# Performance work log

Measured on AMD Instinct MI355X. Metric: run time of the kernel, lower is better.

## Reference

```python
import jax, jax.numpy as jnp
import numpy as np


def _lstm_layer(x_seq, w_ih, w_hh, b_ih, b_hh):
    """One LSTM layer, batch_first x_seq [B,T,D]; PyTorch gate order i,f,g,o."""
    B, T, _ = x_seq.shape
    H = w_hh.shape[1]
    # precompute input contribution for all timesteps: [B,T,4H]
    xg = jnp.einsum('btd,gd->btg', x_seq, w_ih) + b_ih + b_hh
    xg_t = jnp.swapaxes(xg, 0, 1)  # [T,B,4H]

    def step(carry, g_in):
        h, c = carry
        g = g_in + h @ w_hh.T  # [B,4H]
        i, f, gg, o = jnp.split(g, 4, axis=-1)
        i = jax.nn.sigmoid(i)
        f = jax.nn.sigmoid(f)
        gg = jnp.tanh(gg)
        o = jax.nn.sigmoid(o)
        c = f * c + i * gg
        h = o * jnp.tanh(c)
        return (h, c), h

    h0 = jnp.zeros((B, H), x_seq.dtype)
    c0 = jnp.zeros((B, H), x_seq.dtype)
    (_, _), hs = jax.lax.scan(step, (h0, c0), xg_t)
    return jnp.swapaxes(hs, 0, 1)  # [B,T,H]


def setup_inputs() -> dict:
    key = jax.random.key(0)
    ks = jax.random.split(key, 12)
    V, E, H, B, T = 50000, 100, 64, 256, 512
    s = 0.1
    emb = jax.random.normal(ks[0], (V, E), jnp.float32) * s
    emb = emb.at[0].set(0.0)  # padding_idx=0
    return {
        'x': jax.random.randint(ks[1], (B, T), 0, V),
        'emb': emb,
        'w_ih0': jax.random.normal(ks[2], (4 * H, E), jnp.float32) * s,
        'w_hh0': jax.random.normal(ks[3], (4 * H, H), jnp.float32) * s,
        'b_ih0': jax.random.normal(ks[4], (4 * H,), jnp.float32) * s,
        'b_hh0': jax.random.normal(ks[5], (4 * H,), jnp.float32) * s,
        'w_ih1': jax.random.normal(ks[6], (4 * H, H), jnp.float32) * s,
        'w_hh1': jax.random.normal(ks[7], (4 * H, H), jnp.float32) * s,
        'b_ih1': jax.random.normal(ks[8], (4 * H,), jnp.float32) * s,
        'b_hh1': jax.random.normal(ks[9], (4 * H,), jnp.float32) * s,
        'fc_w': jax.random.normal(ks[10], (1, H), jnp.float32) * s,
        'fc_b': jax.random.normal(ks[11], (1,), jnp.float32) * s,
    }


def reference(x, emb, w_ih0, w_hh0, b_ih0, b_hh0,
              w_ih1, w_hh1, b_ih1, b_hh1, fc_w, fc_b):
    emb_eff = emb.at[0].set(0.0)  # padding_idx=0 row stays zero
    embedded = emb_eff[x]  # [B,T,E]
    h1 = _lstm_layer(embedded, w_ih0, w_hh0, b_ih0, b_hh0)
    h2 = _lstm_layer(h1, w_ih1, w_hh1, b_ih1, b_hh1)
    last = h2[:, -1, :]  # [B,H]
    # eval mode: dropout is identity
    act = jax.nn.relu(last)
    out = act @ fc_w.T + fc_b  # [B,1]
    return jax.nn.sigmoid(out)
```

## Files before the change

kernel.cpp:

```cpp
#include <hip/hip_runtime.h>

#define VSZ 50000
#define ESZ 100
#define HSZ 64
#define GSZ 256
#define BSZ 256
#define TSZ 512

__device__ __forceinline__ float fast_rcp(float x) { return __builtin_amdgcn_rcpf(x); }
__device__ __forceinline__ float sigmoid_f(float x) { return fast_rcp(1.f + __expf(-x)); }
__device__ __forceinline__ float tanh_f(float x) {
    float e = __expf(2.f * x);
    return 1.f - 2.f * fast_rcp(e + 1.f);
}

__global__ __launch_bounds__(256) void build_table(
    const float* __restrict__ emb, const float* __restrict__ w_ih0,
    const float* __restrict__ b_ih0, const float* __restrict__ b_hh0,
    float* __restrict__ Gt)
{
    const int g = threadIdx.x;
    const int row0 = blockIdx.x * 32;
    const int col = ((g & 63) << 2) + (g >> 6);

    float w[ESZ];
    #pragma unroll
    for (int e = 0; e < ESZ; e += 4) {
        float4 v = *(const float4*)(w_ih0 + g * ESZ + e);
        w[e] = v.x; w[e + 1] = v.y; w[e + 2] = v.z; w[e + 3] = v.w;
    }
    const float bias = b_ih0[g] + b_hh0[g];

    #pragma unroll 1
    for (int r = row0; r < row0 + 32 && r < VSZ; r += 2) {
        const int off0 = __builtin_amdgcn_readfirstlane(r * ESZ);
        const float* e0 = emb + off0;
        const float* e1 = e0 + ESZ;
        float a0 = bias, a1 = 0.f, a2 = 0.f, a3 = 0.f;
        float b0 = bias, b1 = 0.f, b2 = 0.f, b3 = 0.f;
        #pragma unroll
        for (int e = 0; e < ESZ; e += 4) {
            a0 += e0[e    ] * w[e    ]; a1 += e0[e + 1] * w[e + 1];
            a2 += e0[e + 2] * w[e + 2]; a3 += e0[e + 3] * w[e + 3];
            b0 += e1[e    ] * w[e    ]; b1 += e1[e + 1] * w[e + 1];
            b2 += e1[e + 2] * w[e + 2]; b3 += e1[e + 3] * w[e + 3];
        }
        Gt[(size_t)r       * GSZ + col] = (a0 + a1) + (a2 + a3);
        Gt[(size_t)(r + 1) * GSZ + col] = (b0 + b1) + (b2 + b3);
    }
}

__device__ __forceinline__ void sync_lds() {
    asm volatile("s_waitcnt lgkmcnt(0)\n\ts_barrier" ::: "memory");
}

#define LD4(ptr, off) (*(const float4*)((ptr) + (off)))
#define K4(v) asm volatile("" : "+v"(v.x), "+v"(v.y), "+v"(v.z), "+v"(v.w))
#define KEEPALL \
  K4(W00);K4(W01);K4(W02);K4(W03);K4(W10);K4(W11);K4(W12);K4(W13); \
  K4(W20);K4(W21);K4(W22);K4(W23);K4(W30);K4(W31);K4(W32);K4(W33); \
  K4(U00);K4(U01);K4(U02);K4(U03);K4(U10);K4(U11);K4(U12);K4(U13); \
  K4(U20);K4(U21);K4(U22);K4(U23);K4(U30);K4(U31);K4(U32);K4(U33)
#define DOTACC(p, W, h) p += W.x*h.x; p += W.y*h.y; p += W.z*h.z; p += W.w*h.w

__global__ __launch_bounds__(512, 2) void lstm_fused(
    const int* __restrict__ x, const float* __restrict__ Gt,
    const float* __restrict__ w_hh0,
    const float* __restrict__ w_ih1, const float* __restrict__ w_hh1,
    const float* __restrict__ b_ih1, const float* __restrict__ b_hh1,
    const float* __restrict__ fc_w, const float* __restrict__ fc_b,
    float* __restrict__ out)
{
    const int tid = threadIdx.x;
    const int b   = blockIdx.x;
    const bool isA = tid < 256;
    const int lt  = tid & 255;
    const int q   = lt >> 2;
    const int j   = lt & 3;

    __shared__ __align__(16) float h0b[2][HSZ];
    __shared__ __align__(16) float h1b[2][HSZ];
    __shared__ int xtok[TSZ];

    const float* bW = (isA ? w_hh0 : w_ih1) + (q * HSZ + 16 * j);
    const float* bU = w_hh1 + (q * HSZ + 16 * j);

    float4 W00=LD4(bW,0),     W01=LD4(bW,4),     W02=LD4(bW,8),     W03=LD4(bW,12);
    float4 W10=LD4(bW,4096),  W11=LD4(bW,4100),  W12=LD4(bW,4104),  W13=LD4(bW,4108);
    float4 W20=LD4(bW,8192),  W21=LD4(bW,8196),  W22=LD4(bW,8200),  W23=LD4(bW,8204);
    float4 W30=LD4(bW,12288), W31=LD4(bW,12292), W32=LD4(bW,12296), W33=LD4(bW,12300);
    float4 U00=LD4(bU,0),     U01=LD4(bU,4),     U02=LD4(bU,8),     U03=LD4(bU,12);
    float4 U10=LD4(bU,4096),  U11=LD4(bU,4100),  U12=LD4(bU,4104),  U13=LD4(bU,4108);
    float4 U20=LD4(bU,8192),  U21=LD4(bU,8196),  U22=LD4(bU,8200),  U23=LD4(bU,8204);
    float4 U30=LD4(bU,12288), U31=LD4(bU,12292), U32=LD4(bU,12296), U33=LD4(bU,12300);

    float bi0 = 0.f, bi1 = 0.f, bi2 = 0.f, bi3 = 0.f;
    if (!isA) {
        bi0 = b_ih1[q]       + b_hh1[q];
        bi1 = b_ih1[64 + q]  + b_hh1[64 + q];
        bi2 = b_ih1[128 + q] + b_hh1[128 + q];
        bi3 = b_ih1[192 + q] + b_hh1[192 + q];
    }

    if (tid < 128)      ((float*)h0b)[tid] = 0.f;
    else if (tid < 256) ((float*)h1b)[tid - 128] = 0.f;
    xtok[tid] = x[b * TSZ + tid];
    __syncthreads();

    float4 xg = LD4(Gt, (size_t)xtok[0] * GSZ + 4 * q);
    float c = 0.f;

    #pragma unroll 1
    for (int k = 0; k <= TSZ; ++k) {
        KEEPALL;

        const int rb = (k ^ 1) & 1;
        const float4* h0v = (const float4*)h0b[rb];
        float4 ha = h0v[j*4+0], hb = h0v[j*4+1], hc = h0v[j*4+2], hd = h0v[j*4+3];
        float p0 = 0.f, p1 = 0.f, p2 = 0.f, p3 = 0.f;
        DOTACC(p0,W00,ha); DOTACC(p0,W01,hb); DOTACC(p0,W02,hc); DOTACC(p0,W03,hd);
        DOTACC(p1,W10,ha); DOTACC(p1,W11,hb); DOTACC(p1,W12,hc); DOTACC(p1,W13,hd);
        DOTACC(p2,W20,ha); DOTACC(p2,W21,hb); DOTACC(p2,W22,hc); DOTACC(p2,W23,hd);
        DOTACC(p3,W30,ha); DOTACC(p3,W31,hb); DOTACC(p3,W32,hc); DOTACC(p3,W33,hd);

        if (!isA && k >= 1) {
            const float4* h1v = (const float4*)h1b[k & 1];
            float4 ea = h1v[j*4+0], eb = h1v[j*4+1], ec = h1v[j*4+2], ed = h1v[j*4+3];
            DOTACC(p0,U00,ea); DOTACC(p0,U01,eb); DOTACC(p0,U02,ec); DOTACC(p0,U03,ed);
            DOTACC(p1,U10,ea); DOTACC(p1,U11,eb); DOTACC(p1,U12,ec); DOTACC(p1,U13,ed);
            DOTACC(p2,U20,ea); DOTACC(p2,U21,eb); DOTACC(p2,U22,ec); DOTACC(p2,U23,ed);
            DOTACC(p3,U30,ea); DOTACC(p3,U31,eb); DOTACC(p3,U32,ec); DOTACC(p3,U33,ed);
        }

        p0 += __shfl_xor(p0, 1, 64); p0 += __shfl_xor(p0, 2, 64);
        p1 += __shfl_xor(p1, 1, 64); p1 += __shfl_xor(p1, 2, 64);
        p2 += __shfl_xor(p2, 1, 64); p2 += __shfl_xor(p2, 2, 64);
        p3 += __shfl_xor(p3, 1, 64); p3 += __shfl_xor(p3, 2, 64);

        if (isA) {
            if (k < TSZ) {
                float4 xg_n;
                const bool pf = (k + 1 < TSZ);
                if (pf) xg_n = LD4(Gt, (size_t)xtok[k + 1] * GSZ + 4 * q);
                float ig = sigmoid_f(p0 + xg.x);
                float fg = sigmoid_f(p1 + xg.y);
                float gg = tanh_f   (p2 + xg.z);
                float og = sigmoid_f(p3 + xg.w);
                c = fg * c + ig * gg;
                float hn = og * tanh_f(c);
                if (j == 0) h0b[k & 1][q] = hn;
                if (pf) xg = xg_n;
            }
        } else {
            if (k >= 1) {
                float ig = sigmoid_f(p0 + bi0);
                float fg = sigmoid_f(p1 + bi1);
                float gg = tanh_f   (p2 + bi2);
                float og = sigmoid_f(p3 + bi3);
                c = fg * c + ig * gg;
                float hn = og * tanh_f(c);
                if (j == 0) h1b[(k ^ 1) & 1][q] = hn;
            }
        }
        sync_lds();
    }

    if (tid < HSZ) {
        float v = fmaxf(h1b[1][tid], 0.f) * fc_w[tid];
        #pragma unroll
        for (int off = 32; off > 0; off >>= 1) v += __shfl_down(v, off, 64);
        if (tid == 0) out[b] = sigmoid_f(v + fc_b[0]);
    }
}

extern "C" void kernel_launch(void* const* d_in, const int* in_sizes, int n_in,
                              void* d_out, int out_size, void* d_ws, size_t ws_size,
                              hipStream_t stream) {
    const int*   x     = (const int*)  d_in[0];
    const float* emb   = (const float*)d_in[1];
    const float* w_ih0 = (const float*)d_in[2];
    const float* w_hh0 = (const float*)d_in[3];
    const float* b_ih0 = (const float*)d_in[4];
    const float* b_hh0 = (const float*)d_in[5];
    const float* w_ih1 = (const float*)d_in[6];
    const float* w_hh1 = (const float*)d_in[7];
    const float* b_ih1 = (const float*)d_in[8];
    const float* b_hh1 = (const float*)d_in[9];
    const float* fc_w  = (const float*)d_in[10];
    const float* fc_b  = (const float*)d_in[11];
    float* out = (float*)d_out;

    float* Gt = (float*)d_ws;

    build_table<<<dim3((VSZ + 31) / 32), dim3(256), 0, stream>>>(
        emb, w_ih0, b_ih0, b_hh0, Gt);
    lstm_fused<<<dim3(BSZ), dim3(512), 0, stream>>>(
        x, Gt, w_hh0, w_ih1, w_hh1, b_ih1, b_hh1, fc_w, fc_b, out);
}
```

Before: 568.4 us.

## Split layer-1 work across 512 threads and distribute gate activations per lane

The fused LSTM kernel grows from 512 to 768 threads. The layer-1 group now uses 8 lanes per hidden unit, each holding half the weights, which cuts per-thread registers and FMA chain length. Each lane now evaluates one gate activation through a unified sigmoid/tanh formula after a butterfly reduction, instead of every lane computing all four. The table-building kernel switches to float4 embedding loads and a different occupancy bound. The cost is extra shuffles per step and larger blocks, which may limit occupancy.

```diff
diff --git a/kernel.cpp b/kernel.cpp
--- a/kernel.cpp
+++ b/kernel.cpp
@@ -14,7 +14,7 @@
     return 1.f - 2.f * fast_rcp(e + 1.f);
 }
 
-__global__ __launch_bounds__(256) void build_table(
+__global__ __launch_bounds__(256, 2) void build_table(
     const float* __restrict__ emb, const float* __restrict__ w_ih0,
     const float* __restrict__ b_ih0, const float* __restrict__ b_hh0,
     float* __restrict__ Gt)
@@ -32,18 +32,23 @@
     const float bias = b_ih0[g] + b_hh0[g];
 
     #pragma unroll 1
-    for (int r = row0; r < row0 + 32 && r < VSZ; r += 2) {
-        const int off0 = __builtin_amdgcn_readfirstlane(r * ESZ);
-        const float* e0 = emb + off0;
+    for (int r = row0; r < row0 + 32; r += 2) {
+        if (r + 1 >= VSZ + 1) break;
+        if (r >= VSZ) break;
+        unsigned long long u0 = (unsigned long long)(emb + (size_t)r * ESZ);
+        asm("" : "+v"(u0));
+        const float* e0 = (const float*)u0;
         const float* e1 = e0 + ESZ;
         float a0 = bias, a1 = 0.f, a2 = 0.f, a3 = 0.f;
         float b0 = bias, b1 = 0.f, b2 = 0.f, b3 = 0.f;
         #pragma unroll
         for (int e = 0; e < ESZ; e += 4) {
-            a0 += e0[e    ] * w[e    ]; a1 += e0[e + 1] * w[e + 1];
-            a2 += e0[e + 2] * w[e + 2]; a3 += e0[e + 3] * w[e + 3];
-            b0 += e1[e    ] * w[e    ]; b1 += e1[e + 1] * w[e + 1];
-            b2 += e1[e + 2] * w[e + 2]; b3 += e1[e + 3] * w[e + 3];
+            float4 u = *(const float4*)(e0 + e);
+            float4 v = *(const float4*)(e1 + e);
+            a0 += u.x * w[e]; a1 += u.y * w[e + 1];
+            a2 += u.z * w[e + 2]; a3 += u.w * w[e + 3];
+            b0 += v.x * w[e]; b1 += v.y * w[e + 1];
+            b2 += v.z * w[e + 2]; b3 += v.w * w[e + 3];
         }
         Gt[(size_t)r       * GSZ + col] = (a0 + a1) + (a2 + a3);
         Gt[(size_t)(r + 1) * GSZ + col] = (b0 + b1) + (b2 + b3);
@@ -55,15 +60,14 @@
 }
 
 #define LD4(ptr, off) (*(const float4*)((ptr) + (off)))
-#define K4(v) asm volatile("" : "+v"(v.x), "+v"(v.y), "+v"(v.z), "+v"(v.w))
-#define KEEPALL \
-  K4(W00);K4(W01);K4(W02);K4(W03);K4(W10);K4(W11);K4(W12);K4(W13); \
-  K4(W20);K4(W21);K4(W22);K4(W23);K4(W30);K4(W31);K4(W32);K4(W33); \
-  K4(U00);K4(U01);K4(U02);K4(U03);K4(U10);K4(U11);K4(U12);K4(U13); \
-  K4(U20);K4(U21);K4(U22);K4(U23);K4(U30);K4(U31);K4(U32);K4(U33)
-#define DOTACC(p, W, h) p += W.x*h.x; p += W.y*h.y; p += W.z*h.z; p += W.w*h.w
-
-__global__ __launch_bounds__(512, 2) void lstm_fused(
+#define PIN4(v) asm("" : "+v"(v.x), "+v"(v.y), "+v"(v.z), "+v"(v.w))
+#define DOT4(acc, Sa, Sb, Sc, Sd)                                  \
+    acc += Sa.x*H0.x; acc += Sa.y*H0.y; acc += Sa.z*H0.z; acc += Sa.w*H0.w; \
+    acc += Sb.x*H1.x; acc += Sb.y*H1.y; acc += Sb.z*H1.z; acc += Sb.w*H1.w; \
+    acc += Sc.x*H2.x; acc += Sc.y*H2.y; acc += Sc.z*H2.z; acc += Sc.w*H2.w; \
+    acc += Sd.x*H3.x; acc += Sd.y*H3.y; acc += Sd.z*H3.z; acc += Sd.w*H3.w
+
+__global__ __launch_bounds__(768, 3) void lstm_fused(
     const int* __restrict__ x, const float* __restrict__ Gt,
     const float* __restrict__ w_hh0,
     const float* __restrict__ w_ih1, const float* __restrict__ w_hh1,
@@ -74,94 +78,99 @@
     const int tid = threadIdx.x;
     const int b   = blockIdx.x;
     const bool isA = tid < 256;
-    const int lt  = tid & 255;
-    const int q   = lt >> 2;
-    const int j   = lt & 3;
+    const int lt  = isA ? tid : (tid - 256);
+    const int q   = isA ? (lt >> 2) : (lt >> 3);
+    const int j   = isA ? (lt & 3) : (lt & 7);
+    const int gt  = j & 3;
 
     __shared__ __align__(16) float h0b[2][HSZ];
     __shared__ __align__(16) float h1b[2][HSZ];
     __shared__ int xtok[TSZ];
 
-    const float* bW = (isA ? w_hh0 : w_ih1) + (q * HSZ + 16 * j);
-    const float* bU = w_hh1 + (q * HSZ + 16 * j);
-
-    float4 W00=LD4(bW,0),     W01=LD4(bW,4),     W02=LD4(bW,8),     W03=LD4(bW,12);
-    float4 W10=LD4(bW,4096),  W11=LD4(bW,4100),  W12=LD4(bW,4104),  W13=LD4(bW,4108);
-    float4 W20=LD4(bW,8192),  W21=LD4(bW,8196),  W22=LD4(bW,8200),  W23=LD4(bW,8204);
-    float4 W30=LD4(bW,12288), W31=LD4(bW,12292), W32=LD4(bW,12296), W33=LD4(bW,12300);
-    float4 U00=LD4(bU,0),     U01=LD4(bU,4),     U02=LD4(bU,8),     U03=LD4(bU,12);
-    float4 U10=LD4(bU,4096),  U11=LD4(bU,4100),  U12=LD4(bU,4104),  U13=LD4(bU,4108);
-    float4 U20=LD4(bU,8192),  U21=LD4(bU,8196),  U22=LD4(bU,8200),  U23=LD4(bU,8204);
-    float4 U30=LD4(bU,12288), U31=LD4(bU,12292), U32=LD4(bU,12296), U33=LD4(bU,12300);
-
-    float bi0 = 0.f, bi1 = 0.f, bi2 = 0.f, bi3 = 0.f;
-    if (!isA) {
-        bi0 = b_ih1[q]       + b_hh1[q];
-        bi1 = b_ih1[64 + q]  + b_hh1[64 + q];
-        bi2 = b_ih1[128 + q] + b_hh1[128 + q];
-        bi3 = b_ih1[192 + q] + b_hh1[192 + q];
-    }
+    const float* pw1 = isA ? (w_hh0 + q * HSZ + 16 * j)
+                           : (w_ih1 + q * HSZ + 8 * j);
+    const float* pw2 = isA ? (w_hh0 + q * HSZ + 16 * j + 8)
+                           : (w_hh1 + q * HSZ + 8 * j);
+
+    float4 S00=LD4(pw1,0),     S01=LD4(pw1,4),     S02=LD4(pw2,0),     S03=LD4(pw2,4);
+    float4 S10=LD4(pw1,4096),  S11=LD4(pw1,4100),  S12=LD4(pw2,4096),  S13=LD4(pw2,4100);
+    float4 S20=LD4(pw1,8192),  S21=LD4(pw1,8196),  S22=LD4(pw2,8192),  S23=LD4(pw2,8196);
+    float4 S30=LD4(pw1,12288), S31=LD4(pw1,12292), S32=LD4(pw2,12288), S33=LD4(pw2,12292);
+    PIN4(S00); PIN4(S01); PIN4(S02); PIN4(S03);
+    PIN4(S10); PIN4(S11); PIN4(S12); PIN4(S13);
+    PIN4(S20); PIN4(S21); PIN4(S22); PIN4(S23);
+    PIN4(S30); PIN4(S31); PIN4(S32); PIN4(S33);
+
+    float addend_b = 0.f;
+    if (!isA) addend_b = b_ih1[gt * HSZ + q] + b_hh1[gt * HSZ + q];
+    const float mco = (gt == 2) ?  2.f : -1.f;
+    const float Aco = (gt == 2) ?  1.f :  0.f;
+    const float Bco = (gt == 2) ? -2.f :  1.f;
 
     if (tid < 128)      ((float*)h0b)[tid] = 0.f;
     else if (tid < 256) ((float*)h1b)[tid - 128] = 0.f;
-    xtok[tid] = x[b * TSZ + tid];
+    if (tid < TSZ) xtok[tid] = x[b * TSZ + tid];
     __syncthreads();
 
-    float4 xg = LD4(Gt, (size_t)xtok[0] * GSZ + 4 * q);
     float c = 0.f;
+    float xg_cur = 0.f;
+    if (isA) xg_cur = Gt[(size_t)xtok[0] * GSZ + 4 * q + j];
 
     #pragma unroll 1
     for (int k = 0; k <= TSZ; ++k) {
-        KEEPALL;
-
-        const int rb = (k ^ 1) & 1;
-        const float4* h0v = (const float4*)h0b[rb];
-        float4 ha = h0v[j*4+0], hb = h0v[j*4+1], hc = h0v[j*4+2], hd = h0v[j*4+3];
-        float p0 = 0.f, p1 = 0.f, p2 = 0.f, p3 = 0.f;
-        DOTACC(p0,W00,ha); DOTACC(p0,W01,hb); DOTACC(p0,W02,hc); DOTACC(p0,W03,hd);
-        DOTACC(p1,W10,ha); DOTACC(p1,W11,hb); DOTACC(p1,W12,hc); DOTACC(p1,W13,hd);
-        DOTACC(p2,W20,ha); DOTACC(p2,W21,hb); DOTACC(p2,W22,hc); DOTACC(p2,W23,hd);
-        DOTACC(p3,W30,ha); DOTACC(p3,W31,hb); DOTACC(p3,W32,hc); DOTACC(p3,W33,hd);
-
-        if (!isA && k >= 1) {
-            const float4* h1v = (const float4*)h1b[k & 1];
-            float4 ea = h1v[j*4+0], eb = h1v[j*4+1], ec = h1v[j*4+2], ed = h1v[j*4+3];
-            DOTACC(p0,U00,ea); DOTACC(p0,U01,eb); DOTACC(p0,U02,ec); DOTACC(p0,U03,ed);
-            DOTACC(p1,U10,ea); DOTACC(p1,U11,eb); DOTACC(p1,U12,ec); DOTACC(p1,U13,ed);
-            DOTACC(p2,U20,ea); DOTACC(p2,U21,eb); DOTACC(p2,U22,ec); DOTACC(p2,U23,ed);
-            DOTACC(p3,U30,ea); DOTACC(p3,U31,eb); DOTACC(p3,U32,ec); DOTACC(p3,U33,ed);
+        float xg_nxt = 0.f;
+        if (isA && k + 1 < TSZ)
+            xg_nxt = Gt[(size_t)xtok[k + 1] * GSZ + 4 * q + j];
+
+        const float4* h0v = (const float4*)h0b[(k ^ 1) & 1];
+        const float4* h1v = (const float4*)h1b[k & 1];
+        const float4* hA  = h0v + (isA ? 4 * j : 2 * j);
+        const float4* hB  = isA ? (h0v + 4 * j + 2) : (h1v + 2 * j);
+        float4 H0 = hA[0], H1 = hA[1], H2 = hB[0], H3 = hB[1];
+
+        float d0 = 0.f, d1 = 0.f, d2 = 0.f, d3 = 0.f;
+        DOT4(d0, S00, S01, S02, S03);
+        DOT4(d1, S10, S11, S12, S13);
+        DOT4(d2, S20, S21, S22, S23);
+        DOT4(d3, S30, S31, S32, S33);
+
+        if (!isA) {
+            d0 += __shfl_xor(d0, 4, 64); d1 += __shfl_xor(d1, 4, 64);
+            d2 += __shfl_xor(d2, 4, 64); d3 += __shfl_xor(d3, 4, 64);
         }
-
-        p0 += __shfl_xor(p0, 1, 64); p0 += __shfl_xor(p0, 2, 64);
-        p1 += __shfl_xor(p1, 1, 64); p1 += __shfl_xor(p1, 2, 64);
-        p2 += __shfl_xor(p2, 1, 64); p2 += __shfl_xor(p2, 2, 64);
-        p3 += __shfl_xor(p3, 1, 64); p3 += __shfl_xor(p3, 2, 64);
-
-        if (isA) {
-            if (k < TSZ) {
-                float4 xg_n;
-                const bool pf = (k + 1 < TSZ);
-                if (pf) xg_n = LD4(Gt, (size_t)xtok[k + 1] * GSZ + 4 * q);
-                float ig = sigmoid_f(p0 + xg.x);
-                float fg = sigmoid_f(p1 + xg.y);
-                float gg = tanh_f   (p2 + xg.z);
-                float og = sigmoid_f(p3 + xg.w);
-                c = fg * c + ig * gg;
-                float hn = og * tanh_f(c);
-                if (j == 0) h0b[k & 1][q] = hn;
-                if (pf) xg = xg_n;
-            }
-        } else {
-            if (k >= 1) {
-                float ig = sigmoid_f(p0 + bi0);
-                float fg = sigmoid_f(p1 + bi1);
-                float gg = tanh_f   (p2 + bi2);
-                float og = sigmoid_f(p3 + bi3);
-                c = fg * c + ig * gg;
-                float hn = og * tanh_f(c);
-                if (j == 0) h1b[(k ^ 1) & 1][q] = hn;
+        const bool lo2 = (j & 2) == 0;
+        float u  = lo2 ? d2 : d0, v = lo2 ? d3 : d1;
+        float ru = __shfl_xor(u, 2, 64), rv = __shfl_xor(v, 2, 64);
+        float aa = (lo2 ? d0 : d2) + ru;
+        float bb = (lo2 ? d1 : d3) + rv;
+        const bool lo1 = (j & 1) == 0;
+        float ws = lo1 ? bb : aa;
+        float rw = __shfl_xor(ws, 1, 64);
+        float s  = (lo1 ? aa : bb) + rw;
+
+        s += isA ? xg_cur : addend_b;
+        float e   = __expf(mco * s);
+        float act = fmaf(Bco, fast_rcp(1.f + e), Aco);
+
+        float o1 = __shfl_xor(act, 1, 64);
+        float ge = lo1 ? act : o1;
+        float go = lo1 ? o1 : act;
+        float pe = __shfl_xor(ge, 2, 64), po = __shfl_xor(go, 2, 64);
+        float iact = lo2 ? ge : pe;
+        float fact = lo2 ? go : po;
+        float gact = lo2 ? pe : ge;
+        float oact = lo2 ? po : go;
+
+        const bool active = isA ? (k < TSZ) : (k >= 1);
+        if (active) {
+            c = fact * c + iact * gact;
+            float hn = oact * tanh_f(c);
+            if (j == 0) {
+                if (isA) h0b[k & 1][q] = hn;
+                else     h1b[(k ^ 1) & 1][q] = hn;
             }
         }
+        xg_cur = xg_nxt;
         sync_lds();
     }
 
@@ -194,6 +203,6 @@
 
     build_table<<<dim3((VSZ + 31) / 32), dim3(256), 0, stream>>>(
         emb, w_ih0, b_ih0, b_hh0, Gt);
-    lstm_fused<<<dim3(BSZ), dim3(512), 0, stream>>>(
+    lstm_fused<<<dim3(BSZ), dim3(768), 0, stream>>>(
         x, Gt, w_hh0, w_ih1, w_hh1, b_ih1, b_hh1, fc_w, fc_b, out);
 }
```

Result: slower. 687.6 us (+21.0%).
